# Optimization experiments

Hardware: AMD Instinct MI355X
Metric: run time of the kernel (lower is better)

Reference implementation:

```python
import jax, jax.numpy as jnp
import numpy as np

B, T, E, H, N_TAGS = 128, 512, 256, 512, 32
START, END = 30, 31


def setup_inputs() -> dict:
    key = jax.random.key(0)
    ks = jax.random.split(key, 12)
    s = 1.0 / np.sqrt(H)

    def w(k, shape):
        return jax.random.normal(k, shape, jnp.float32) * s

    X = jax.random.normal(ks[0], (B, T, E), jnp.float32)
    length = jnp.sort(jax.random.randint(ks[1], (B,), T // 2, T + 1))[::-1]
    masks = (jnp.arange(T)[None, :] < length[:, None]).astype(jnp.float32)
    W_ih_f, W_hh_f, b_f = w(ks[2], (4 * H, E)), w(ks[3], (4 * H, H)), w(ks[4], (4 * H,))
    W_ih_b, W_hh_b, b_b = w(ks[5], (4 * H, E)), w(ks[6], (4 * H, H)), w(ks[7], (4 * H,))
    W_out, b_out = w(ks[8], (N_TAGS, 2 * H)), w(ks[9], (N_TAGS,))
    transitions = jax.random.normal(ks[10], (N_TAGS, N_TAGS), jnp.float32)
    transitions = transitions.at[:, START].set(-1e4).at[END, :].set(-1e4)
    return dict(X=X, masks=masks, length=length,
                W_ih_f=W_ih_f, W_hh_f=W_hh_f, b_f=b_f,
                W_ih_b=W_ih_b, W_hh_b=W_hh_b, b_b=b_b,
                W_out=W_out, b_out=b_out, transitions=transitions)


def _lstm_dir(Xt, mt, Wih, Whh, b, reverse):
    # Xt: [T,B,E], mt: [T,B,1]. Masked update emulates pack_padded_sequence
    # (state frozen on pad; for reverse dir, state stays zero until last valid token).
    h0 = jnp.zeros((Xt.shape[1], H), Xt.dtype)

    def step(carry, inp):
        h, c = carry
        x, m = inp
        gates = x @ Wih.T + h @ Whh.T + b  # [B,4H], torch gate order i,f,g,o
        i, f, g, o = jnp.split(gates, 4, axis=-1)
        i, f, o = jax.nn.sigmoid(i), jax.nn.sigmoid(f), jax.nn.sigmoid(o)
        g = jnp.tanh(g)
        c_new = f * c + i * g
        h_new = o * jnp.tanh(c_new)
        h = m * h_new + (1.0 - m) * h
        c = m * c_new + (1.0 - m) * c
        return (h, c), h

    _, hs = jax.lax.scan(step, (h0, h0), (Xt, mt), reverse=reverse)
    return hs  # [T,B,H]


def reference(X, masks, length, W_ih_f, W_hh_f, b_f, W_ih_b, W_hh_b, b_b, W_out, b_out, transitions):
    Xt = X.transpose(1, 0, 2)            # [T,B,E]
    mT = masks.T                          # [T,B]
    mt = mT[:, :, None]
    hf = _lstm_dir(Xt, mt, W_ih_f, W_hh_f, b_f, False)
    hb = _lstm_dir(Xt, mt, W_ih_b, W_hh_b, b_b, True)
    emis = jnp.concatenate([hf, hb], axis=-1) @ W_out.T + b_out  # [T,B,n_tags]

    # Viterbi forward recurrence with masking
    alphas0 = emis[0] + transitions[START]  # [B,n]

    def vstep(alphas, inp):
        e, m = inp  # e: [B,n], m: [B,1]
        scores = alphas[:, :, None] + transitions[None] + e[:, None, :]  # [B,from,to]
        alphas = m * scores.max(axis=1) + (1.0 - m) * alphas
        return alphas, jnp.argmax(scores, axis=1)

    alphas, bps = jax.lax.scan(vstep, alphas0, (emis[1:], mt[1:]))
    final = alphas + transitions[:, END]
    max_end_scores = final.max(axis=1)      # [B]
    end_tags = jnp.argmax(final, axis=1)    # [B]

    # Masked backtrace: bps[k] is the backpointer into position k+1
    def bstep(cur, inp):
        bp, m = inp  # bp: [B,n], m: [B]
        prev = jnp.where(m > 0, jnp.take_along_axis(bp, cur[:, None], axis=1)[:, 0], cur)
        return prev, prev

    _, outs = jax.lax.scan(bstep, end_tags, (bps, mT[1:]), reverse=True)  # outs[k]=tag at pos k
    tags = jnp.concatenate([outs, end_tags[None]], axis=0).T              # [B,T]
    tags = jnp.where(masks > 0, tags, -1)
    return max_end_scores, tags
```

## Files before the change

kernel.cpp:

```cpp
#include <hip/hip_runtime.h>
#include <cfloat>
#include <cmath>

#define Bn 128
#define Tn 512
#define En 256
#define Hn 512
#define NTAGS 32
#define CHK 64
#define NCHK 12
#define LDW 132
#define WPAD 20

#define OFF_HF 0
#define OFF_HB 131072
#define OFF_CF 262144
#define OFF_CB 327680
#define OFF_EF 393216
#define OFF_EB 2490368

__global__ __launch_bounds__(512, 2) void lstm_step_k(
    const float* __restrict__ X, const float* __restrict__ masks,
    const float* __restrict__ Wih_f, const float* __restrict__ Whh_f, const float* __restrict__ bias_f,
    const float* __restrict__ Wih_b, const float* __restrict__ Whh_b, const float* __restrict__ bias_b,
    const float* __restrict__ Wout, float* __restrict__ ws, int s)
{
  __shared__ __align__(16) float WT[768 * WPAD];
  __shared__ __align__(16) float HX[2][CHK * LDW];
  __shared__ __align__(16) float GL[Bn * 17];
  __shared__ __align__(16) float WoL[512];
  __shared__ __align__(16) float RS[16 * 32];

  const int tid   = threadIdx.x;
  const int blk   = blockIdx.x;
  const int lane  = tid & 63;
  const int wid   = __builtin_amdgcn_readfirstlane(tid >> 6);
  const int cg    = wid & 1;
  const int kt    = wid >> 1;
  const int bg    = lane & 31;
  const int khalf = lane >> 5;

  const int dir = blk >> 7;
  const int bbk = blk & 127;
  const int t = dir ? (Tn - 1 - s) : s;
  const float* Wih  = dir ? Wih_b  : Wih_f;
  const float* Whh  = dir ? Whh_b  : Whh_f;
  const float* bias = dir ? bias_b : bias_f;
  float* hbuf = ws + (dir ? OFF_HB : OFF_HF);
  float* cbuf = ws + (dir ? OFF_CB : OFF_CF);
  const int rbuf = (s + 1) & 1;
  const int wbuf = s & 1;
  const float* hprev = hbuf + rbuf * (Hn * Bn);
  float*       hnext = hbuf + wbuf * (Hn * Bn);
  const int hidx0 = bbk * 4;

  const int etag = bbk & 31;
  const int ebq  = bbk >> 5;

  {
    const int lc = tid & 15;
    const int kw = tid >> 4;
    const int row = (lc >> 2) * Hn + hidx0 + (lc & 3);
    #pragma unroll
    for (int i = 0; i < 6; ++i) {
      const int k = (kw + i * 32) * 4;
      float4 w4;
      if (k < Hn) w4 = *(const float4*)&Whh[(size_t)row * Hn + k];
      else        w4 = *(const float4*)&Wih[(size_t)row * En + (k - Hn)];
      WT[(k + 0) * WPAD + lc] = w4.x; WT[(k + 1) * WPAD + lc] = w4.y;
      WT[(k + 2) * WPAD + lc] = w4.z; WT[(k + 3) * WPAD + lc] = w4.w;
    }
  }
  if (tid < 128) {
    const float4 wo = *(const float4*)&Wout[(size_t)etag * (2 * Hn) + dir * Hn + tid * 4];
    *(float4*)&WoL[tid * 4] = wo;
  }
  {
    #pragma unroll
    for (int r = 0; r < 4; ++r) {
      const int item = r * 512 + tid;
      const float4 v = *(const float4*)&hprev[item * 4];
      const int k = item >> 5;
      const int g = item & 31;
      *(float4*)&HX[0][k * LDW + g * 4] = v;
    }
  }
  __syncthreads();

  float acc[4][8];
  #pragma unroll
  for (int m = 0; m < 4; ++m)
    #pragma unroll
    for (int n = 0; n < 8; ++n) acc[m][n] = 0.f;
  float eacc = 0.f;

  const int xbq = tid & 127;
  const int xeg = tid >> 7;

  #pragma unroll 1
  for (int c = 0; c < NCHK; ++c) {
    const int nxt = c + 1;
    float4 st[4];
    if (nxt < 8) {
      const float* src = hprev + nxt * (CHK * Bn);
      #pragma unroll
      for (int r = 0; r < 4; ++r)
        st[r] = *(const float4*)&src[(r * 512 + tid) * 4];
    } else if (nxt < NCHK) {
      const int e0 = (nxt - 8) * CHK;
      #pragma unroll
      for (int r = 0; r < 4; ++r)
        st[r] = *(const float4*)&X[(size_t)xbq * (Tn * En) + (size_t)t * En + e0 + xeg * 16 + r * 4];
    }

    {
      const float* HXc = &HX[c & 1][0];
      #pragma unroll
      for (int j = 0; j < 8; ++j) {
        const int l = kt * 16 + j * 2 + khalf;
        const float4 av = *(const float4*)&HXc[l * LDW + bg * 4];
        const float4 wa = *(const float4*)&WT[(c * 64 + l) * WPAD + cg * 8];
        const float4 wb = *(const float4*)&WT[(c * 64 + l) * WPAD + cg * 8 + 4];
        const float avf[4] = {av.x, av.y, av.z, av.w};
        const float wvf[8] = {wa.x, wa.y, wa.z, wa.w, wb.x, wb.y, wb.z, wb.w};
        #pragma unroll
        for (int m = 0; m < 4; ++m)
          #pragma unroll
          for (int n = 0; n < 8; ++n)
            acc[m][n] += avf[m] * wvf[n];
      }
      if (c < 8) {
        const int be = tid & 31;
        const int kq = tid >> 5;
        #pragma unroll
        for (int j = 0; j < 4; ++j)
          eacc += HXc[(kq * 4 + j) * LDW + ebq * 32 + be] * WoL[c * 64 + kq * 4 + j];
      }
    }

    if (nxt < 8) {
      float* dst = &HX[nxt & 1][0];
      #pragma unroll
      for (int r = 0; r < 4; ++r) {
        const int item = r * 512 + tid;
        const int k = item >> 5;
        const int g = item & 31;
        *(float4*)&dst[k * LDW + g * 4] = st[r];
      }
    } else if (nxt < NCHK) {
      float* dst = &HX[nxt & 1][0];
      #pragma unroll
      for (int r = 0; r < 4; ++r) {
        const int el = xeg * 16 + r * 4;
        dst[(el + 0) * LDW + xbq] = st[r].x;
        dst[(el + 1) * LDW + xbq] = st[r].y;
        dst[(el + 2) * LDW + xbq] = st[r].z;
        dst[(el + 3) * LDW + xbq] = st[r].w;
      }
    }
    __syncthreads();
  }

  float* P = &HX[0][0];
  const int ks = kt * 2 + khalf;
  #pragma unroll
  for (int n = 0; n < 8; ++n)
    *(float4*)&P[ks * 2048 + (cg * 8 + n) * 128 + bg * 4] =
        make_float4(acc[0][n], acc[1][n], acc[2][n], acc[3][n]);
  RS[(tid >> 5) * 32 + (tid & 31)] = eacc;
  __syncthreads();
  {
    const int b  = tid & 127;
    const int cq = tid >> 7;
    float g4[4] = {0.f, 0.f, 0.f, 0.f};
    #pragma unroll
    for (int k2 = 0; k2 < 8; ++k2)
      #pragma unroll
      for (int ci = 0; ci < 4; ++ci)
        g4[ci] += P[k2 * 2048 + (cq * 4 + ci) * 128 + b];
    #pragma unroll
    for (int ci = 0; ci < 4; ++ci)
      GL[b * 17 + cq * 4 + ci] = g4[ci];
  }
  __syncthreads();

  {
    const int b  = tid & 127;
    const int hh = tid >> 7;
    const int hidx = hidx0 + hh;
    const float gi = GL[b * 17 + hh]      + bias[hidx];
    const float gf = GL[b * 17 + 4 + hh]  + bias[Hn + hidx];
    const float gc = GL[b * 17 + 8 + hh]  + bias[2 * Hn + hidx];
    const float go = GL[b * 17 + 12 + hh] + bias[3 * Hn + hidx];
    const float iv = 1.f / (1.f + expf(-gi));
    const float fv = 1.f / (1.f + expf(-gf));
    const float gv = tanhf(gc);
    const float ov = 1.f / (1.f + expf(-go));
    const float cold = cbuf[hidx * Bn + b];
    const float cnew = fv * cold + iv * gv;
    const float hold = hprev[hidx * Bn + b];
    const float hnew = ov * tanhf(cnew);
    const float m = masks[(size_t)b * Tn + t];
    hnext[hidx * Bn + b] = (m > 0.f) ? hnew : hold;
    cbuf[hidx * Bn + b]  = (m > 0.f) ? cnew : cold;
  }

  if (tid < 32 && s > 0) {
    const int tprev = dir ? (Tn - s) : (s - 1);
    float* Edst = ws + (dir ? OFF_EB : OFF_EF);
    float v = 0.f;
    #pragma unroll
    for (int g = 0; g < 16; ++g) v += RS[g * 32 + tid];
    Edst[(size_t)tprev * (NTAGS * Bn) + etag * Bn + ebq * 32 + tid] = v;
  }
}

__global__ __launch_bounds__(512) void emis_final_k(const float* __restrict__ Wout,
                                                    float* __restrict__ ws)
{
  __shared__ float RSf[16 * Bn];
  const int tid = threadIdx.x;
  const int dir = blockIdx.x >> 5;
  const int tag = blockIdx.x & 31;
  const float* hsrc = ws + (dir ? OFF_HB : OFF_HF) + 1 * (Hn * Bn);
  const int tprev = dir ? 0 : (Tn - 1);
  const float* wrow = Wout + (size_t)tag * (2 * Hn) + dir * Hn;
  float* Edst = ws + (dir ? OFF_EB : OFF_EF);
  const int bq = tid & 31;
  const int kg = tid >> 5;
  float4 a4 = make_float4(0.f, 0.f, 0.f, 0.f);
  #pragma unroll 4
  for (int kk = 0; kk < 32; ++kk) {
    const int k = kg * 32 + kk;
    const float w = wrow[k];
    const float4 h4 = *(const float4*)&hsrc[k * Bn + bq * 4];
    a4.x += h4.x * w; a4.y += h4.y * w; a4.z += h4.z * w; a4.w += h4.w * w;
  }
  *(float4*)&RSf[kg * Bn + bq * 4] = a4;
  __syncthreads();
  if (tid < 128) {
    float v = 0.f;
    #pragma unroll
    for (int g = 0; g < 16; ++g) v += RSf[g * Bn + tid];
    Edst[(size_t)tprev * (NTAGS * Bn) + tag * Bn + tid] = v;
  }
}

__global__ __launch_bounds__(64) void viterbi_k(
    const float* __restrict__ Ef, const float* __restrict__ Eb,
    const float* __restrict__ bout, const float* __restrict__ trans,
    const float* __restrict__ masks, float* __restrict__ out)
{
  const int b = blockIdx.x;
  const int l = threadIdx.x;
  __shared__ float tr[32][32];
  __shared__ float al[32];
  __shared__ float msk[512];
  __shared__ unsigned char bp[512][32];
  __shared__ int tseq[512];

  for (int i = l; i < 1024; i += 64) tr[i >> 5][i & 31] = trans[i];
  for (int i = l; i < 512; i += 64) msk[i] = masks[(size_t)b * 512 + i];
  __syncthreads();

  const int j  = l & 31;
  const int hi = l >> 5;
  if (l < 32)
    al[j] = Ef[(size_t)j * Bn + b] + Eb[(size_t)j * Bn + b] + bout[j] + tr[30][j];
  __syncthreads();

  for (int t = 1; t < 512; ++t) {
    float pmax = -FLT_MAX; int pidx = 0;
    #pragma unroll
    for (int ii = 0; ii < 16; ++ii) {
      const int i = hi * 16 + ii;
      const float sc = al[i] + tr[i][j];
      if (sc > pmax) { pmax = sc; pidx = i; }
    }
    const float omax = __shfl_down(pmax, 32);
    const int   oidx = __shfl_down(pidx, 32);
    if (l < 32) {
      if (omax > pmax) { pmax = omax; pidx = oidx; }
      bp[t][j] = (unsigned char)pidx;
      const float e = Ef[(size_t)t * (NTAGS * Bn) + j * Bn + b]
                    + Eb[(size_t)t * (NTAGS * Bn) + j * Bn + b] + bout[j];
      const float na = pmax + e;
      if (msk[t] > 0.f) al[j] = na;
    }
    __syncthreads();
  }

  float fv; int fidx;
  if (l < 32) { fv = al[l] + tr[l][31]; fidx = l; }
  else        { fv = -FLT_MAX; fidx = 1 << 30; }
  #pragma unroll
  for (int off = 16; off >= 1; off >>= 1) {
    const float v2 = __shfl_xor(fv, off);
    const int   i2 = __shfl_xor(fidx, off);
    if (v2 > fv || (v2 == fv && i2 < fidx)) { fv = v2; fidx = i2; }
  }
  if (l == 0) {
    out[b] = fv;
    int cur = fidx;
    tseq[511] = cur;
    for (int t = 511; t >= 1; --t) {
      const int prev = (msk[t] > 0.f) ? (int)bp[t][cur] : cur;
      tseq[t - 1] = prev;
      cur = prev;
    }
  }
  __syncthreads();
  for (int t = l; t < 512; t += 64) {
    const float tv = (msk[t] > 0.f) ? (float)tseq[t] : -1.0f;
    out[Bn + (size_t)b * 512 + t] = tv;
  }
}

extern "C" void kernel_launch(void* const* d_in, const int* in_sizes, int n_in,
                              void* d_out, int out_size, void* d_ws, size_t ws_size,
                              hipStream_t stream) {
  const float* X      = (const float*)d_in[0];
  const float* masks  = (const float*)d_in[1];
  const float* Wih_f  = (const float*)d_in[3];
  const float* Whh_f  = (const float*)d_in[4];
  const float* bf     = (const float*)d_in[5];
  const float* Wih_b  = (const float*)d_in[6];
  const float* Whh_b  = (const float*)d_in[7];
  const float* bb     = (const float*)d_in[8];
  const float* Wout   = (const float*)d_in[9];
  const float* bout   = (const float*)d_in[10];
  const float* trans  = (const float*)d_in[11];
  float* ws  = (float*)d_ws;
  float* out = (float*)d_out;

  hipMemsetAsync(d_ws, 0, (size_t)OFF_EF * sizeof(float), stream);

  for (int s = 0; s < Tn; ++s)
    lstm_step_k<<<256, 512, 0, stream>>>(X, masks, Wih_f, Whh_f, bf,
                                         Wih_b, Whh_b, bb, Wout, ws, s);
  emis_final_k<<<64, 512, 0, stream>>>(Wout, ws);
  viterbi_k<<<128, 64, 0, stream>>>(ws + OFF_EF, ws + OFF_EB, bout, trans, masks, out);
}
```

Baseline: 11.37 ms.

## Replace per-timestep LSTM launches with persistent kernel and grid barrier

Replaces the 512 per-step kernel launches with one persistent kernel that loops over timesteps and synchronises all 256 blocks through a two-level atomic grid barrier. Weights stay in LDS across steps, the cell state and bias move into registers, and X for the next step is prefetched during the current step with the X chunks processed before the h chunks. This removes launch overhead and repeated weight reloads, but relies on all 256 blocks being co-resident and adds barrier spin latency each step.

Result: slower. 29.08 ms (+155.8%).

```diff
diff --git a/kernel.cpp b/kernel.cpp
--- a/kernel.cpp
+++ b/kernel.cpp
@@ -7,26 +7,45 @@
 #define En 256
 #define Hn 512
 #define NTAGS 32
-#define CHK 64
-#define NCHK 12
 #define LDW 132
 #define WPAD 20
 
 #define OFF_HF 0
 #define OFF_HB 131072
-#define OFF_CF 262144
-#define OFF_CB 327680
-#define OFF_EF 393216
-#define OFF_EB 2490368
-
-__global__ __launch_bounds__(512, 2) void lstm_step_k(
+#define OFF_BAR 262144
+#define OFF_EF 263168
+#define OFF_EB (OFF_EF + Tn * NTAGS * Bn)
+
+__device__ __forceinline__ void gridbar(unsigned* bar, int blk, int tid, unsigned target) {
+  __syncthreads();
+  if (tid == 0) {
+    __threadfence();
+    unsigned* phase = bar;
+    unsigned* root  = bar + 32;
+    unsigned* gcnt  = bar + 64 + ((blk >> 4) << 5);
+    unsigned o = __hip_atomic_fetch_add(gcnt, 1u, __ATOMIC_ACQ_REL, __HIP_MEMORY_SCOPE_AGENT);
+    if (o == 15u) {
+      __hip_atomic_store(gcnt, 0u, __ATOMIC_RELAXED, __HIP_MEMORY_SCOPE_AGENT);
+      unsigned r = __hip_atomic_fetch_add(root, 1u, __ATOMIC_ACQ_REL, __HIP_MEMORY_SCOPE_AGENT);
+      if (r == 15u) {
+        __hip_atomic_store(root, 0u, __ATOMIC_RELAXED, __HIP_MEMORY_SCOPE_AGENT);
+        __hip_atomic_fetch_add(phase, 1u, __ATOMIC_RELEASE, __HIP_MEMORY_SCOPE_AGENT);
+      }
+    }
+    while (__hip_atomic_load(phase, __ATOMIC_ACQUIRE, __HIP_MEMORY_SCOPE_AGENT) < target)
+      __builtin_amdgcn_s_sleep(2);
+  }
+  __syncthreads();
+}
+
+__global__ __launch_bounds__(512, 2) void lstm_persist_k(
     const float* __restrict__ X, const float* __restrict__ masks,
     const float* __restrict__ Wih_f, const float* __restrict__ Whh_f, const float* __restrict__ bias_f,
     const float* __restrict__ Wih_b, const float* __restrict__ Whh_b, const float* __restrict__ bias_b,
-    const float* __restrict__ Wout, float* __restrict__ ws, int s)
+    const float* __restrict__ Wout, float* __restrict__ ws)
 {
   __shared__ __align__(16) float WT[768 * WPAD];
-  __shared__ __align__(16) float HX[2][CHK * LDW];
+  __shared__ __align__(16) float HX[2][64 * LDW];
   __shared__ __align__(16) float GL[Bn * 17];
   __shared__ __align__(16) float WoL[512];
   __shared__ __align__(16) float RS[16 * 32];
@@ -42,18 +61,13 @@
 
   const int dir = blk >> 7;
   const int bbk = blk & 127;
-  const int t = dir ? (Tn - 1 - s) : s;
   const float* Wih  = dir ? Wih_b  : Wih_f;
   const float* Whh  = dir ? Whh_b  : Whh_f;
   const float* bias = dir ? bias_b : bias_f;
   float* hbuf = ws + (dir ? OFF_HB : OFF_HF);
-  float* cbuf = ws + (dir ? OFF_CB : OFF_CF);
-  const int rbuf = (s + 1) & 1;
-  const int wbuf = s & 1;
-  const float* hprev = hbuf + rbuf * (Hn * Bn);
-  float*       hnext = hbuf + wbuf * (Hn * Bn);
+  float* Edst = ws + (dir ? OFF_EB : OFF_EF);
+  unsigned* bar = (unsigned*)(ws + OFF_BAR);
   const int hidx0 = bbk * 4;
-
   const int etag = bbk & 31;
   const int ebq  = bbk >> 5;
 
@@ -75,143 +89,178 @@
     const float4 wo = *(const float4*)&Wout[(size_t)etag * (2 * Hn) + dir * Hn + tid * 4];
     *(float4*)&WoL[tid * 4] = wo;
   }
-  {
-    #pragma unroll
-    for (int r = 0; r < 4; ++r) {
-      const int item = r * 512 + tid;
-      const float4 v = *(const float4*)&hprev[item * 4];
-      const int k = item >> 5;
-      const int g = item & 31;
-      *(float4*)&HX[0][k * LDW + g * 4] = v;
-    }
-  }
-  __syncthreads();
-
-  float acc[4][8];
-  #pragma unroll
-  for (int m = 0; m < 4; ++m)
-    #pragma unroll
-    for (int n = 0; n < 8; ++n) acc[m][n] = 0.f;
-  float eacc = 0.f;
+
+  const int pb = tid & 127;
+  const int ph = tid >> 7;
+  const int hidx = hidx0 + ph;
+  const float bi = bias[hidx];
+  const float bff = bias[Hn + hidx];
+  const float bgg = bias[2 * Hn + hidx];
+  const float bo = bias[3 * Hn + hidx];
+  float c_reg = 0.f, h_reg = 0.f;
 
   const int xbq = tid & 127;
   const int xeg = tid >> 7;
+  const size_t xrow = (size_t)xbq * (Tn * En);
+
+  float4 xA[8];
+  {
+    const int t0 = dir ? (Tn - 1) : 0;
+    #pragma unroll
+    for (int r = 0; r < 8; ++r)
+      xA[r] = *(const float4*)&X[xrow + (size_t)t0 * En + (r >> 2) * 64 + xeg * 16 + (r & 3) * 4];
+  }
 
   #pragma unroll 1
-  for (int c = 0; c < NCHK; ++c) {
-    const int nxt = c + 1;
+  for (int s = 0; s < Tn; ++s) {
+    const int t = dir ? (Tn - 1 - s) : s;
+    const float* hprev = hbuf + ((s + 1) & 1) * (Hn * Bn);
+    float*       hnext = hbuf + (s & 1) * (Hn * Bn);
+    const float mval = masks[(size_t)pb * Tn + t];
+
+    #pragma unroll
+    for (int r = 0; r < 4; ++r) {
+      const int el = xeg * 16 + r * 4;
+      HX[0][(el + 0) * LDW + xbq] = xA[r].x;
+      HX[0][(el + 1) * LDW + xbq] = xA[r].y;
+      HX[0][(el + 2) * LDW + xbq] = xA[r].z;
+      HX[0][(el + 3) * LDW + xbq] = xA[r].w;
+    }
+    __syncthreads();
+
+    float4 xB[8];
+    #pragma unroll
+    for (int r = 0; r < 8; ++r)
+      xB[r] = *(const float4*)&X[xrow + (size_t)t * En + 128 + (r >> 2) * 64 + xeg * 16 + (r & 3) * 4];
+
+    float acc[4][8];
+    #pragma unroll
+    for (int m = 0; m < 4; ++m)
+      #pragma unroll
+      for (int n = 0; n < 8; ++n) acc[m][n] = 0.f;
+    float eacc = 0.f;
     float4 st[4];
-    if (nxt < 8) {
-      const float* src = hprev + nxt * (CHK * Bn);
+
+    #pragma unroll 1
+    for (int c = 0; c < 12; ++c) {
+      const int nxt = c + 1;
+      if (nxt >= 4 && nxt < 12) {
+        const float* src = hprev + (nxt - 4) * (64 * Bn);
+        #pragma unroll
+        for (int r = 0; r < 4; ++r)
+          st[r] = *(const float4*)&src[(r * 512 + tid) * 4];
+      }
+      if (c == 11 && s < Tn - 1) {
+        const int tn = dir ? (Tn - 2 - s) : (s + 1);
+        #pragma unroll
+        for (int r = 0; r < 8; ++r)
+          xA[r] = *(const float4*)&X[xrow + (size_t)tn * En + (r >> 2) * 64 + xeg * 16 + (r & 3) * 4];
+      }
+
+      {
+        const float* HXc = &HX[c & 1][0];
+        const int wk0 = (c < 4) ? (512 + c * 64) : ((c - 4) * 64);
+        #pragma unroll
+        for (int j = 0; j < 8; ++j) {
+          const int l = kt * 16 + j * 2 + khalf;
+          const float4 av = *(const float4*)&HXc[l * LDW + bg * 4];
+          const float4 wa = *(const float4*)&WT[(wk0 + l) * WPAD + cg * 8];
+          const float4 wb = *(const float4*)&WT[(wk0 + l) * WPAD + cg * 8 + 4];
+          const float avf[4] = {av.x, av.y, av.z, av.w};
+          const float wvf[8] = {wa.x, wa.y, wa.z, wa.w, wb.x, wb.y, wb.z, wb.w};
+          #pragma unroll
+          for (int m = 0; m < 4; ++m)
+            #pragma unroll
+            for (int n = 0; n < 8; ++n)
+              acc[m][n] += avf[m] * wvf[n];
+        }
+        if (s > 0 && c >= 4) {
+          const int be = tid & 31;
+          const int kq = tid >> 5;
+          #pragma unroll
+          for (int j = 0; j < 4; ++j)
+            eacc += HXc[(kq * 4 + j) * LDW + ebq * 32 + be] * WoL[(c - 4) * 64 + kq * 4 + j];
+        }
+      }
+
+      if (nxt == 1) {
+        #pragma unroll
+        for (int r = 0; r < 4; ++r) {
+          const int el = xeg * 16 + r * 4;
+          HX[1][(el + 0) * LDW + xbq] = xA[4 + r].x;
+          HX[1][(el + 1) * LDW + xbq] = xA[4 + r].y;
+          HX[1][(el + 2) * LDW + xbq] = xA[4 + r].z;
+          HX[1][(el + 3) * LDW + xbq] = xA[4 + r].w;
+        }
+      } else if (nxt == 2 || nxt == 3) {
+        float* dst = &HX[nxt & 1][0];
+        const int o = (nxt - 2) * 4;
+        #pragma unroll
+        for (int r = 0; r < 4; ++r) {
+          const int el = xeg * 16 + r * 4;
+          dst[(el + 0) * LDW + xbq] = xB[o + r].x;
+          dst[(el + 1) * LDW + xbq] = xB[o + r].y;
+          dst[(el + 2) * LDW + xbq] = xB[o + r].z;
+          dst[(el + 3) * LDW + xbq] = xB[o + r].w;
+        }
+      } else if (nxt >= 4 && nxt < 12) {
+        float* dst = &HX[nxt & 1][0];
+        #pragma unroll
+        for (int r = 0; r < 4; ++r) {
+          const int item = r * 512 + tid;
+          *(float4*)&dst[(item >> 5) * LDW + (item & 31) * 4] = st[r];
+        }
+      }
+      __syncthreads();
+    }
+
+    float* P = &HX[0][0];
+    const int ks = kt * 2 + khalf;
+    #pragma unroll
+    for (int n = 0; n < 8; ++n)
+      *(float4*)&P[ks * 2048 + (cg * 8 + n) * 128 + bg * 4] =
+          make_float4(acc[0][n], acc[1][n], acc[2][n], acc[3][n]);
+    RS[(tid >> 5) * 32 + (tid & 31)] = eacc;
+    __syncthreads();
+    {
+      const int b  = tid & 127;
+      const int cq = tid >> 7;
+      float g4[4] = {0.f, 0.f, 0.f, 0.f};
       #pragma unroll
-      for (int r = 0; r < 4; ++r)
-        st[r] = *(const float4*)&src[(r * 512 + tid) * 4];
-    } else if (nxt < NCHK) {
-      const int e0 = (nxt - 8) * CHK;
-      #pragma unroll
-      for (int r = 0; r < 4; ++r)
-        st[r] = *(const float4*)&X[(size_t)xbq * (Tn * En) + (size_t)t * En + e0 + xeg * 16 + r * 4];
-    }
-
-    {
-      const float* HXc = &HX[c & 1][0];
-      #pragma unroll
-      for (int j = 0; j < 8; ++j) {
-        const int l = kt * 16 + j * 2 + khalf;
-        const float4 av = *(const float4*)&HXc[l * LDW + bg * 4];
-        const float4 wa = *(const float4*)&WT[(c * 64 + l) * WPAD + cg * 8];
-        const float4 wb = *(const float4*)&WT[(c * 64 + l) * WPAD + cg * 8 + 4];
-        const float avf[4] = {av.x, av.y, av.z, av.w};
-        const float wvf[8] = {wa.x, wa.y, wa.z, wa.w, wb.x, wb.y, wb.z, wb.w};
-        #pragma unroll
-        for (int m = 0; m < 4; ++m)
-          #pragma unroll
-          for (int n = 0; n < 8; ++n)
-            acc[m][n] += avf[m] * wvf[n];
-      }
-      if (c < 8) {
-        const int be = tid & 31;
-        const int kq = tid >> 5;
-        #pragma unroll
-        for (int j = 0; j < 4; ++j)
-          eacc += HXc[(kq * 4 + j) * LDW + ebq * 32 + be] * WoL[c * 64 + kq * 4 + j];
-      }
-    }
-
-    if (nxt < 8) {
-      float* dst = &HX[nxt & 1][0];
-      #pragma unroll
-      for (int r = 0; r < 4; ++r) {
-        const int item = r * 512 + tid;
-        const int k = item >> 5;
-        const int g = item & 31;
-        *(float4*)&dst[k * LDW + g * 4] = st[r];
-      }
-    } else if (nxt < NCHK) {
-      float* dst = &HX[nxt & 1][0];
-      #pragma unroll
-      for (int r = 0; r < 4; ++r) {
-        const int el = xeg * 16 + r * 4;
-        dst[(el + 0) * LDW + xbq] = st[r].x;
-        dst[(el + 1) * LDW + xbq] = st[r].y;
-        dst[(el + 2) * LDW + xbq] = st[r].z;
-        dst[(el + 3) * LDW + xbq] = st[r].w;
-      }
-    }
-    __syncthreads();
-  }
-
-  float* P = &HX[0][0];
-  const int ks = kt * 2 + khalf;
-  #pragma unroll
-  for (int n = 0; n < 8; ++n)
-    *(float4*)&P[ks * 2048 + (cg * 8 + n) * 128 + bg * 4] =
-        make_float4(acc[0][n], acc[1][n], acc[2][n], acc[3][n]);
-  RS[(tid >> 5) * 32 + (tid & 31)] = eacc;
-  __syncthreads();
-  {
-    const int b  = tid & 127;
-    const int cq = tid >> 7;
-    float g4[4] = {0.f, 0.f, 0.f, 0.f};
-    #pragma unroll
-    for (int k2 = 0; k2 < 8; ++k2)
+      for (int k2 = 0; k2 < 8; ++k2)
+        #pragma unroll
+        for (int ci = 0; ci < 4; ++ci)
+          g4[ci] += P[k2 * 2048 + (cq * 4 + ci) * 128 + b];
       #pragma unroll
       for (int ci = 0; ci < 4; ++ci)
-        g4[ci] += P[k2 * 2048 + (cq * 4 + ci) * 128 + b];
-    #pragma unroll
-    for (int ci = 0; ci < 4; ++ci)
-      GL[b * 17 + cq * 4 + ci] = g4[ci];
-  }
-  __syncthreads();
-
-  {
-    const int b  = tid & 127;
-    const int hh = tid >> 7;
-    const int hidx = hidx0 + hh;
-    const float gi = GL[b * 17 + hh]      + bias[hidx];
-    const float gf = GL[b * 17 + 4 + hh]  + bias[Hn + hidx];
-    const float gc = GL[b * 17 + 8 + hh]  + bias[2 * Hn + hidx];
-    const float go = GL[b * 17 + 12 + hh] + bias[3 * Hn + hidx];
-    const float iv = 1.f / (1.f + expf(-gi));
-    const float fv = 1.f / (1.f + expf(-gf));
-    const float gv = tanhf(gc);
-    const float ov = 1.f / (1.f + expf(-go));
-    const float cold = cbuf[hidx * Bn + b];
-    const float cnew = fv * cold + iv * gv;
-    const float hold = hprev[hidx * Bn + b];
-    const float hnew = ov * tanhf(cnew);
-    const float m = masks[(size_t)b * Tn + t];
-    hnext[hidx * Bn + b] = (m > 0.f) ? hnew : hold;
-    cbuf[hidx * Bn + b]  = (m > 0.f) ? cnew : cold;
-  }
-
-  if (tid < 32 && s > 0) {
-    const int tprev = dir ? (Tn - s) : (s - 1);
-    float* Edst = ws + (dir ? OFF_EB : OFF_EF);
-    float v = 0.f;
-    #pragma unroll
-    for (int g = 0; g < 16; ++g) v += RS[g * 32 + tid];
-    Edst[(size_t)tprev * (NTAGS * Bn) + etag * Bn + ebq * 32 + tid] = v;
+        GL[b * 17 + cq * 4 + ci] = g4[ci];
+    }
+    __syncthreads();
+
+    {
+      const float gi = GL[pb * 17 + ph]       + bi;
+      const float gf = GL[pb * 17 + 4 + ph]   + bff;
+      const float gc = GL[pb * 17 + 8 + ph]   + bgg;
+      const float go = GL[pb * 17 + 12 + ph]  + bo;
+      const float iv = 1.f / (1.f + expf(-gi));
+      const float fv = 1.f / (1.f + expf(-gf));
+      const float gv = tanhf(gc);
+      const float ov = 1.f / (1.f + expf(-go));
+      const float cnew = fv * c_reg + iv * gv;
+      const float hnew = ov * tanhf(cnew);
+      if (mval > 0.f) { h_reg = hnew; c_reg = cnew; }
+      hnext[hidx * Bn + pb] = h_reg;
+    }
+
+    if (tid < 32 && s > 0) {
+      const int tprev = dir ? (Tn - s) : (s - 1);
+      float v = 0.f;
+      #pragma unroll
+      for (int g = 0; g < 16; ++g) v += RS[g * 32 + tid];
+      Edst[(size_t)tprev * (NTAGS * Bn) + etag * Bn + ebq * 32 + tid] = v;
+    }
+
+    gridbar(bar, blk, tid, (unsigned)(s + 1));
   }
 }
 
@@ -335,9 +384,8 @@
 
   hipMemsetAsync(d_ws, 0, (size_t)OFF_EF * sizeof(float), stream);
 
-  for (int s = 0; s < Tn; ++s)
-    lstm_step_k<<<256, 512, 0, stream>>>(X, masks, Wih_f, Whh_f, bf,
-                                         Wih_b, Whh_b, bb, Wout, ws, s);
+  lstm_persist_k<<<256, 512, 0, stream>>>(X, masks, Wih_f, Whh_f, bf,
+                                          Wih_b, Whh_b, bb, Wout, ws);
   emis_final_k<<<64, 512, 0, stream>>>(Wout, ws);
   viterbi_k<<<128, 64, 0, stream>>>(ws + OFF_EF, ws + OFF_EB, bout, trans, masks, out);
 }
```
